# Kernel optimization log

Hardware: AMD Instinct MI355X
Metric: run time of the kernel (lower is better)

## Reference

```python
import jax, jax.numpy as jnp
import numpy as np

B, S, D, H = 2, 2048, 1024, 16
HD = D // H
EPS = 1e-5


def _layernorm(x, g, b):
    mu = jnp.mean(x, axis=-1, keepdims=True)
    var = jnp.mean(jnp.square(x - mu), axis=-1, keepdims=True)
    return (x - mu) * jax.lax.rsqrt(var + EPS) * g + b


def setup_inputs() -> dict:
    key = jax.random.key(0)
    ks = jax.random.split(key, 12)
    s = 1.0 / np.sqrt(D)
    return {
        "x": jax.random.normal(ks[0], (B, S, D), jnp.float32),
        "Wq": jax.random.uniform(ks[1], (D, D), jnp.float32, -s, s),
        "bq": jax.random.uniform(ks[2], (D,), jnp.float32, -s, s),
        "Wk": jax.random.uniform(ks[3], (D, D), jnp.float32, -s, s),
        "bk": jax.random.uniform(ks[4], (D,), jnp.float32, -s, s),
        "Wv": jax.random.uniform(ks[5], (D, D), jnp.float32, -s, s),
        "bv": jax.random.uniform(ks[6], (D,), jnp.float32, -s, s),
        "ln_g": jnp.ones((D,), jnp.float32),
        "ln_b": jnp.zeros((D,), jnp.float32),
        "W1": jax.random.uniform(ks[7], (D, D), jnp.float32, -s, s),
        "b1": jax.random.uniform(ks[8], (D,), jnp.float32, -s, s),
        "W2": jax.random.uniform(ks[9], (D, D), jnp.float32, -s, s),
        "b2": jax.random.uniform(ks[10], (D,), jnp.float32, -s, s),
    }


def reference(x, Wq, bq, Wk, bk, Wv, bv, ln_g, ln_b, W1, b1, W2, b2):
    # QKV projections (torch Linear: x @ W.T + b), split into heads -> [B,H,S,HD]
    q = (x @ Wq.T + bq).reshape(B, S, H, HD).transpose(0, 2, 1, 3)
    k = (x @ Wk.T + bk).reshape(B, S, H, HD).transpose(0, 2, 1, 3)
    v = (x @ Wv.T + bv).reshape(B, S, H, HD).transpose(0, 2, 1, 3)
    # Full score matrix [B,H,S,S] (faithful to unfused original)
    scores = jnp.einsum("bhqd,bhkd->bhqk", q, k) / np.sqrt(HD).astype(np.float32)
    attn = jax.nn.softmax(scores, axis=-1)  # dropout = identity (eval mode)
    ctx = jnp.einsum("bhqk,bhkd->bhqd", attn, v)
    ctx = ctx.transpose(0, 2, 1, 3).reshape(B, S, D)
    ctx = _layernorm(ctx + x, ln_g, ln_b)
    ffn = jax.nn.relu(ctx @ W1.T + b1) @ W2.T + b2
    return _layernorm(ffn + ctx, ln_g, ln_b)
```

## Files before the change

### kernel.cpp

```cpp
#include <hip/hip_runtime.h>
#include <stdint.h>

#define D_MODEL 1024
#define NHEAD   16
#define HDIM    64
#define BATCH   2
#define SEQ     2048
#define NTOK    (BATCH*SEQ)

typedef unsigned short u16;
typedef unsigned int   u32;
typedef __attribute__((ext_vector_type(8)))  short bf16x8;
typedef __attribute__((ext_vector_type(8)))  u16   u16x8;
typedef __attribute__((ext_vector_type(4)))  u16   u16x4;
typedef __attribute__((ext_vector_type(4)))  u32   u32x4;
typedef __attribute__((ext_vector_type(4)))  float f32x4;
typedef __attribute__((ext_vector_type(16))) float f32x16;

#if __has_builtin(__builtin_amdgcn_exp2f)
#define EXP2F __builtin_amdgcn_exp2f
#else
#define EXP2F exp2f
#endif

__device__ __forceinline__ u16 f2bf(float f) {
  uint32_t u = __float_as_uint(f);
  u += 0x7fffu + ((u >> 16) & 1u);
  return (u16)(u >> 16);
}

__device__ __forceinline__ void gl_lds16(const u16* g, u16* l) {
  __builtin_amdgcn_global_load_lds(
      (const __attribute__((address_space(1))) void*)g,
      (__attribute__((address_space(3))) void*)l, 16, 0, 0);
}

__device__ __forceinline__ u32 cvtpk(float lo, float hi) {
  u32 r;
  asm("v_cvt_pk_bf16_f32 %0, %1, %2" : "=v"(r) : "v"(lo), "v"(hi));
  return r;
}
__device__ __forceinline__ void pl32swap(u32& a, u32& b) {
  asm("v_permlane32_swap_b32 %0, %1" : "+v"(a), "+v"(b));
}

__device__ __forceinline__ f32x16 mfma32(bf16x8 a, bf16x8 b, f32x16 c) {
  return __builtin_amdgcn_mfma_f32_32x32x16_bf16(a, b, c, 0, 0, 0);
}

__global__ __launch_bounds__(256) void cvt_all(
    const float* __restrict__ x,  const float* __restrict__ Wq,
    const float* __restrict__ Wk, const float* __restrict__ Wv,
    const float* __restrict__ W1, const float* __restrict__ W2,
    const float* __restrict__ bq, const float* __restrict__ bk,
    const float* __restrict__ bv,
    u16* __restrict__ x_bf, u16* __restrict__ wqkv,
    u16* __restrict__ w1b,  u16* __restrict__ w2b,
    float* __restrict__ bqkv) {
  const int bid = blockIdx.x, t = threadIdx.x;
  if (bid == 4608) {
    for (int i = t; i < 3072; i += 256)
      bqkv[i] = i < 1024 ? bq[i] : (i < 2048 ? bk[i - 1024] : bv[i - 2048]);
    return;
  }
  const float* src; u16* dst; int off;
  if (bid < 2048)      { src = x;  dst = x_bf;            off = bid; }
  else if (bid < 2560) { src = Wq; dst = wqkv;            off = bid - 2048; }
  else if (bid < 3072) { src = Wk; dst = wqkv + (1 << 20); off = bid - 2560; }
  else if (bid < 3584) { src = Wv; dst = wqkv + (2 << 20); off = bid - 3072; }
  else if (bid < 4096) { src = W1; dst = w1b;             off = bid - 3584; }
  else                 { src = W2; dst = w2b;             off = bid - 4096; }
  const int i = (off * 256 + t) * 8;
  float4 a = *(const float4*)(src + i);
  float4 b = *(const float4*)(src + i + 4);
  u16x8 o;
  o[0] = f2bf(a.x); o[1] = f2bf(a.y); o[2] = f2bf(a.z); o[3] = f2bf(a.w);
  o[4] = f2bf(b.x); o[5] = f2bf(b.y); o[6] = f2bf(b.z); o[7] = f2bf(b.w);
  *(u16x8*)(dst + i) = o;
}

template <int EPI>
__global__ __launch_bounds__(256) void gemm_bt(const u16* __restrict__ A,
                                               const u16* __restrict__ B,
                                               const float* __restrict__ bias,
                                               void* __restrict__ C,
                                               int M, int N, int K) {
  __shared__ u16 a_lds[2][128 * 32];
  __shared__ u16 b_lds[2][128 * 32];
  const int t = threadIdx.x;
  const int l = t & 63;
  const int w = t >> 6;
  const int wr = w >> 1, wc = w & 1;
  const int gxn = N >> 7;
  const int cpx = gridDim.x >> 3;
  const int swz = (blockIdx.x & 7) * cpx + (blockIdx.x >> 3);
  const int bm = (swz / gxn) * 128, bn = (swz % gxn) * 128;
  const int fl = l & 15, fh = l >> 4;

  f32x4 acc[4][4] = {};

  const int row0 = t >> 2;
  const int row1 = (t + 256) >> 2;
  const int col0 = (t & 3) * 8;

#define GSTAGE(bb, kk)                                                         \
  gl_lds16(A + (size_t)(bm + row0) * K + (kk) + col0, &a_lds[bb][t * 8]);      \
  gl_lds16(A + (size_t)(bm + row1) * K + (kk) + col0,                          \
           &a_lds[bb][(t + 256) * 8]);                                         \
  gl_lds16(B + (size_t)(bn + row0) * K + (kk) + col0, &b_lds[bb][t * 8]);      \
  gl_lds16(B + (size_t)(bn + row1) * K + (kk) + col0,                          \
           &b_lds[bb][(t + 256) * 8]);

  GSTAGE(0, 0);
  __syncthreads();
  int cur = 0;

  for (int k0 = 0; k0 < K; k0 += 32) {
    if (k0 + 32 < K) { GSTAGE(cur ^ 1, k0 + 32); }

    bf16x8 af[4], bf[4];
#pragma unroll
    for (int mi = 0; mi < 4; ++mi)
      af[mi] = *(const bf16x8*)&a_lds[cur][(wr * 64 + mi * 16 + fl) * 32 + fh * 8];
#pragma unroll
    for (int ni = 0; ni < 4; ++ni)
      bf[ni] = *(const bf16x8*)&b_lds[cur][(wc * 64 + ni * 16 + fl) * 32 + fh * 8];
#pragma unroll
    for (int mi = 0; mi < 4; ++mi)
#pragma unroll
      for (int ni = 0; ni < 4; ++ni)
        acc[mi][ni] = __builtin_amdgcn_mfma_f32_16x16x32_bf16(
            af[mi], bf[ni], acc[mi][ni], 0, 0, 0);

    __syncthreads();
    cur ^= 1;
  }
#undef GSTAGE

#pragma unroll
  for (int mi = 0; mi < 4; ++mi) {
#pragma unroll
    for (int ni = 0; ni < 4; ++ni) {
      const int col = bn + wc * 64 + ni * 16 + fl;
      const float bv = bias ? bias[col] : 0.f;
#pragma unroll
      for (int r = 0; r < 4; ++r) {
        const int row = bm + wr * 64 + mi * 16 + fh * 4 + r;
        float v = acc[mi][ni][r] + bv;
        if (EPI == 0) {
          ((float*)C)[(size_t)row * N + col] = v;
        } else if (EPI == 1) {
          ((u16*)C)[(size_t)row * N + col] = f2bf(v);
        } else {
          ((u16*)C)[(size_t)row * N + col] = f2bf(fmaxf(v, 0.f));
        }
      }
    }
  }
}

__global__ __launch_bounds__(256) void transpose_v(const u16* __restrict__ qkv,
                                                   u16* __restrict__ vT) {
  __shared__ u16 tile[64][72];
  const int t = threadIdx.x;
  const int s0 = blockIdx.x * 64;
  const int bh = blockIdx.y, b = bh >> 4, h = bh & 15;
#pragma unroll
  for (int cc = 0; cc < 2; ++cc) {
    int idx = t + cc * 256, row = idx >> 3, c = idx & 7;
    *(bf16x8*)&tile[row][c * 8] = *(const bf16x8*)(
        qkv + (size_t)(b * SEQ + s0 + row) * 3072 + 2048 + h * 64 + c * 8);
  }
  __syncthreads();
#pragma unroll
  for (int cc = 0; cc < 2; ++cc) {
    int idx = t + cc * 256, drow = idx >> 3, c = idx & 7;
    u16x8 o;
#pragma unroll
    for (int j = 0; j < 8; ++j) o[j] = tile[c * 8 + j][drow];
    *(u16x8*)(vT + (size_t)(bh * 64 + drow) * SEQ + s0 + c * 8) = o;
  }
}

__global__ __launch_bounds__(256, 4) void attn_kernel(const u16* __restrict__ qkv,
                                                      const u16* __restrict__ vT,
                                                      float* __restrict__ ctx) {
  __shared__ u16 smem[4][64 * 64];
  __shared__ float mlbuf[2][2][32];

  const int t = threadIdx.x, l = t & 63, w = t >> 6;
  const int r0 = l & 31, hi = l >> 5, hib = hi * 16;
  const int qg = w >> 1, hfv = w & 1;

  const int id = blockIdx.x;
  const int swz = (id & 7) * 128 + (id >> 3);
  const int qblk = swz & 31;
  const int bh = swz >> 5;
  const int b = bh >> 4, h = bh & 15;
  const int q0 = qblk * 64;
  const size_t rowbase = (size_t)b * SEQ;

  bf16x8 qf[4];
#pragma unroll
  for (int kd = 0; kd < 4; ++kd)
    qf[kd] = *(const bf16x8*)(qkv +
        (rowbase + q0 + qg * 32 + r0) * 3072 + h * 64 + kd * 16 + hi * 8);

  f32x16 acc[2] = {};
  f32x16 lsum = {};
  const float C = 0.18033688011f;
  const float SM0 = 20.0f * C;
  const short ONEB = (short)0x3F80;
  const bf16x8 ones = {ONEB, ONEB, ONEB, ONEB, ONEB, ONEB, ONEB, ONEB};

  const u16* kb = smem[hfv * 2 + 0];
  const u16* vb = smem[hfv * 2 + 1];

  for (int s = 0; s < 16; ++s) {
    __syncthreads();
#pragma unroll
    for (int cc = 0; cc < 8; ++cc) {
      const int i = t + cc * 256;
      const int arr = i >> 9;
      const int j = i & 511;
      const int rr = j >> 3, cb = (j & 7) * 16;
      const int sc_ = cb ^ ((rr & 7) << 4);
      const int hv = arr >> 1;
      u16* dst = &smem[arr][j * 8];
      if ((arr & 1) == 0)
        gl_lds16(qkv + (rowbase + hv * 1024 + s * 64 + rr) * 3072 + 1024 +
                     h * 64 + (sc_ >> 1), dst);
      else
        gl_lds16(vT + ((size_t)bh * 64 + rr) * SEQ + hv * 1024 + s * 64 +
                     (sc_ >> 1), dst);
    }
    __syncthreads();

    f32x16 p0 = {}, p1 = {};
    __builtin_amdgcn_s_setprio(1);
#pragma unroll
    for (int kd = 0; kd < 4; ++kd) {
      const int cb = kd * 32 + hib;
      const uint8_t* pk = (const uint8_t*)kb;
      bf16x8 klo = *(const bf16x8*)(pk + r0 * 128 + (cb ^ ((r0 & 7) << 4)));
      bf16x8 khi = *(const bf16x8*)(pk + (r0 + 32) * 128 + (cb ^ ((r0 & 7) << 4)));
      p0 = mfma32(klo, qf[kd], p0);
      p1 = mfma32(khi, qf[kd], p1);
    }
    __builtin_amdgcn_s_setprio(0);

#pragma unroll
    for (int i = 0; i < 16; ++i) {
      p0[i] = EXP2F(fmaf(p0[i], C, -SM0));
      p1[i] = EXP2F(fmaf(p1[i], C, -SM0));
    }

    bf16x8 pb[4];
    {
      u32 c0, c1, c2, c3;
      u32x4 f;
      c0 = cvtpk(p0[0], p0[1]);   c1 = cvtpk(p0[2], p0[3]);
      c2 = cvtpk(p0[4], p0[5]);   c3 = cvtpk(p0[6], p0[7]);
      pl32swap(c0, c2); pl32swap(c1, c3);
      f[0] = c0; f[1] = c1; f[2] = c2; f[3] = c3; pb[0] = *(bf16x8*)&f;
      c0 = cvtpk(p0[8], p0[9]);   c1 = cvtpk(p0[10], p0[11]);
      c2 = cvtpk(p0[12], p0[13]); c3 = cvtpk(p0[14], p0[15]);
      pl32swap(c0, c2); pl32swap(c1, c3);
      f[0] = c0; f[1] = c1; f[2] = c2; f[3] = c3; pb[1] = *(bf16x8*)&f;
      c0 = cvtpk(p1[0], p1[1]);   c1 = cvtpk(p1[2], p1[3]);
      c2 = cvtpk(p1[4], p1[5]);   c3 = cvtpk(p1[6], p1[7]);
      pl32swap(c0, c2); pl32swap(c1, c3);
      f[0] = c0; f[1] = c1; f[2] = c2; f[3] = c3; pb[2] = *(bf16x8*)&f;
      c0 = cvtpk(p1[8], p1[9]);   c1 = cvtpk(p1[10], p1[11]);
      c2 = cvtpk(p1[12], p1[13]); c3 = cvtpk(p1[14], p1[15]);
      pl32swap(c0, c2); pl32swap(c1, c3);
      f[0] = c0; f[1] = c1; f[2] = c2; f[3] = c3; pb[3] = *(bf16x8*)&f;
    }

    __builtin_amdgcn_s_setprio(1);
#pragma unroll
    for (int ks = 0; ks < 4; ++ks)
      lsum = mfma32(ones, pb[ks], lsum);
#pragma unroll
    for (int dblk = 0; dblk < 2; ++dblk) {
#pragma unroll
      for (int ks = 0; ks < 4; ++ks) {
        const int rr = dblk * 32 + r0;
        const int cb = ks * 32 + hib;
        bf16x8 vf = *(const bf16x8*)((const uint8_t*)vb + rr * 128 +
                                     (cb ^ ((rr & 7) << 4)));
        acc[dblk] = mfma32(vf, pb[ks], acc[dblk]);
      }
    }
    __builtin_amdgcn_s_setprio(0);
  }

  if (hi == 0) mlbuf[qg][hfv][r0] = lsum[0];
  __syncthreads();

  float* os = (float*)smem + qg * 32 * 68;
  if (hfv == 0) {
#pragma unroll
    for (int dblk = 0; dblk < 2; ++dblk)
#pragma unroll
      for (int i = 0; i < 16; ++i) {
        const int d = dblk * 32 + (i & 3) + 8 * (i >> 2) + 4 * hi;
        os[r0 * 68 + d] = acc[dblk][i];
      }
  }
  __syncthreads();
  if (hfv == 1) {
#pragma unroll
    for (int dblk = 0; dblk < 2; ++dblk)
#pragma unroll
      for (int i = 0; i < 16; ++i) {
        const int d = dblk * 32 + (i & 3) + 8 * (i >> 2) + 4 * hi;
        os[r0 * 68 + d] += acc[dblk][i];
      }
#pragma unroll
    for (int it = 0; it < 8; ++it) {
      const int r = it * 4 + (l >> 4);
      const int c = (l & 15) * 4;
      const float inv = 1.f / (mlbuf[qg][0][r] + mlbuf[qg][1][r]);
      float4 v = *(const float4*)&os[r * 68 + c];
      v.x *= inv; v.y *= inv; v.z *= inv; v.w *= inv;
      *(float4*)&ctx[(rowbase + q0 + qg * 32 + r) * D_MODEL + h * 64 + c] = v;
    }
  }
}

__global__ __launch_bounds__(256) void ln_kernel(const float* __restrict__ a,
                                                 const float* __restrict__ res,
                                                 const float* __restrict__ g,
                                                 const float* __restrict__ bta,
                                                 float* __restrict__ outf,
                                                 u16* __restrict__ outb) {
  __shared__ float sbuf[4];
  const int t = threadIdx.x;
  const size_t row = blockIdx.x;
  const float4 va = *(const float4*)(a + row * 1024 + t * 4);
  const float4 vr = *(const float4*)(res + row * 1024 + t * 4);
  float v[4] = {va.x + vr.x, va.y + vr.y, va.z + vr.z, va.w + vr.w};
  float s = v[0] + v[1] + v[2] + v[3];
#pragma unroll
  for (int m = 32; m; m >>= 1) s += __shfl_xor(s, m, 64);
  if ((t & 63) == 0) sbuf[t >> 6] = s;
  __syncthreads();
  const float mean = (sbuf[0] + sbuf[1] + sbuf[2] + sbuf[3]) * (1.f / 1024.f);
  float q = 0.f;
#pragma unroll
  for (int i = 0; i < 4; ++i) { v[i] -= mean; q += v[i] * v[i]; }
#pragma unroll
  for (int m = 32; m; m >>= 1) q += __shfl_xor(q, m, 64);
  __syncthreads();
  if ((t & 63) == 0) sbuf[t >> 6] = q;
  __syncthreads();
  const float var = (sbuf[0] + sbuf[1] + sbuf[2] + sbuf[3]) * (1.f / 1024.f);
  const float rs = rsqrtf(var + 1e-5f);
  const float4 vg = *(const float4*)(g + t * 4);
  const float4 vb = *(const float4*)(bta + t * 4);
  float o[4];
  o[0] = v[0] * rs * vg.x + vb.x;
  o[1] = v[1] * rs * vg.y + vb.y;
  o[2] = v[2] * rs * vg.z + vb.z;
  o[3] = v[3] * rs * vg.w + vb.w;
  float4 of = {o[0], o[1], o[2], o[3]};
  *(float4*)(outf + row * 1024 + t * 4) = of;
  if (outb) {
    u16x4 ob;
#pragma unroll
    for (int i = 0; i < 4; ++i) ob[i] = f2bf(o[i]);
    *(u16x4*)(outb + row * 1024 + t * 4) = ob;
  }
}

extern "C" void kernel_launch(void* const* d_in, const int* in_sizes, int n_in,
                              void* d_out, int out_size, void* d_ws, size_t ws_size,
                              hipStream_t stream) {
  const float* x    = (const float*)d_in[0];
  const float* Wq   = (const float*)d_in[1];
  const float* bq   = (const float*)d_in[2];
  const float* Wk   = (const float*)d_in[3];
  const float* bk   = (const float*)d_in[4];
  const float* Wv   = (const float*)d_in[5];
  const float* bv   = (const float*)d_in[6];
  const float* ln_g = (const float*)d_in[7];
  const float* ln_b = (const float*)d_in[8];
  const float* W1   = (const float*)d_in[9];
  const float* b1   = (const float*)d_in[10];
  const float* W2   = (const float*)d_in[11];
  const float* b2   = (const float*)d_in[12];
  float* out = (float*)d_out;

  uint8_t* ws = (uint8_t*)d_ws;
  const size_t MB = 1 << 20;
  u16*   x_bf  = (u16*)  (ws + 0 * MB);
  u16*   wqkv  = (u16*)  (ws + 8 * MB);
  u16*   w1b   = (u16*)  (ws + 14 * MB);
  u16*   w2b   = (u16*)  (ws + 16 * MB);
  float* bqkv  = (float*)(ws + 18 * MB);
  u16*   qkv   = (u16*)  (ws + 19 * MB);
  u16*   vT    = (u16*)  (ws + 43 * MB);
  float* ctx   = (float*)(ws + 51 * MB);
  float* y     = (float*)(ws + 67 * MB);
  u16*   y_bf  = (u16*)  (ws + 83 * MB);
  u16*   h1    = (u16*)  (ws + 91 * MB);
  float* ffn   = (float*)(ws + 99 * MB);

  cvt_all<<<4609, 256, 0, stream>>>(x, Wq, Wk, Wv, W1, W2, bq, bk, bv,
                                    x_bf, wqkv, w1b, w2b, bqkv);
  gemm_bt<1><<<768, 256, 0, stream>>>(x_bf, wqkv, bqkv, qkv, NTOK, 3072, 1024);
  transpose_v<<<dim3(32, 32), 256, 0, stream>>>(qkv, vT);
  attn_kernel<<<1024, 256, 0, stream>>>(qkv, vT, ctx);
  ln_kernel<<<4096, 256, 0, stream>>>(ctx, x, ln_g, ln_b, y, y_bf);
  gemm_bt<2><<<256, 256, 0, stream>>>(y_bf, w1b, b1, h1, NTOK, 1024, 1024);
  gemm_bt<0><<<256, 256, 0, stream>>>(h1, w2b, b2, ffn, NTOK, 1024, 1024);
  ln_kernel<<<4096, 256, 0, stream>>>(ffn, y, ln_g, ln_b, out, nullptr);
}
```

Measured before the change: 270.5 us.

## Deepen GEMM global-to-LDS pipeline to four stages with explicit vmcnt waits

```diff
diff --git a/kernel.cpp b/kernel.cpp
--- a/kernel.cpp
+++ b/kernel.cpp
@@ -85,8 +85,8 @@
                                                const float* __restrict__ bias,
                                                void* __restrict__ C,
                                                int M, int N, int K) {
-  __shared__ u16 a_lds[2][128 * 32];
-  __shared__ u16 b_lds[2][128 * 32];
+  __shared__ u16 a_lds[4][128 * 32];
+  __shared__ u16 b_lds[4][128 * 32];
   const int t = threadIdx.x;
   const int l = t & 63;
   const int w = t >> 6;
@@ -96,46 +96,62 @@
   const int swz = (blockIdx.x & 7) * cpx + (blockIdx.x >> 3);
   const int bm = (swz / gxn) * 128, bn = (swz % gxn) * 128;
   const int fl = l & 15, fh = l >> 4;
+  const int NT = K >> 5;
 
   f32x4 acc[4][4] = {};
 
-  const int row0 = t >> 2;
-  const int row1 = (t + 256) >> 2;
-  const int col0 = (t & 3) * 8;
-
-#define GSTAGE(bb, kk)                                                         \
-  gl_lds16(A + (size_t)(bm + row0) * K + (kk) + col0, &a_lds[bb][t * 8]);      \
-  gl_lds16(A + (size_t)(bm + row1) * K + (kk) + col0,                          \
-           &a_lds[bb][(t + 256) * 8]);                                         \
-  gl_lds16(B + (size_t)(bn + row0) * K + (kk) + col0, &b_lds[bb][t * 8]);      \
-  gl_lds16(B + (size_t)(bn + row1) * K + (kk) + col0,                          \
-           &b_lds[bb][(t + 256) * 8]);
-
-  GSTAGE(0, 0);
-  __syncthreads();
-  int cur = 0;
-
-  for (int k0 = 0; k0 < K; k0 += 32) {
-    if (k0 + 32 < K) { GSTAGE(cur ^ 1, k0 + 32); }
-
-    bf16x8 af[4], bf[4];
-#pragma unroll
-    for (int mi = 0; mi < 4; ++mi)
-      af[mi] = *(const bf16x8*)&a_lds[cur][(wr * 64 + mi * 16 + fl) * 32 + fh * 8];
-#pragma unroll
-    for (int ni = 0; ni < 4; ++ni)
-      bf[ni] = *(const bf16x8*)&b_lds[cur][(wc * 64 + ni * 16 + fl) * 32 + fh * 8];
-#pragma unroll
-    for (int mi = 0; mi < 4; ++mi)
-#pragma unroll
-      for (int ni = 0; ni < 4; ++ni)
-        acc[mi][ni] = __builtin_amdgcn_mfma_f32_16x16x32_bf16(
-            af[mi], bf[ni], acc[mi][ni], 0, 0, 0);
-
-    __syncthreads();
-    cur ^= 1;
-  }
-#undef GSTAGE
+  const int srow = t >> 2;
+  const int scol = (t & 3) * 8;
+
+#define STG(bb, kt)                                                            \
+  {                                                                            \
+    gl_lds16(A + (size_t)(bm + srow) * K + (kt) * 32 + scol,                   \
+             &a_lds[bb][t * 8]);                                               \
+    gl_lds16(A + (size_t)(bm + 64 + srow) * K + (kt) * 32 + scol,              \
+             &a_lds[bb][(t + 256) * 8]);                                       \
+    gl_lds16(B + (size_t)(bn + srow) * K + (kt) * 32 + scol,                   \
+             &b_lds[bb][t * 8]);                                               \
+    gl_lds16(B + (size_t)(bn + 64 + srow) * K + (kt) * 32 + scol,              \
+             &b_lds[bb][(t + 256) * 8]);                                       \
+  }
+
+  STG(0, 0);
+  STG(1, 1);
+  STG(2, 2);
+
+#define KBODY(tt, VMS)                                                         \
+  {                                                                            \
+    __builtin_amdgcn_sched_barrier(0);                                         \
+    if ((tt) + 3 < NT) STG(((tt) + 3) & 3, (tt) + 3);                          \
+    asm volatile("s_waitcnt vmcnt(" VMS ")" ::: "memory");                     \
+    __builtin_amdgcn_sched_barrier(0);                                         \
+    __builtin_amdgcn_s_barrier();                                              \
+    __builtin_amdgcn_sched_barrier(0);                                         \
+    const u16* ap = a_lds[(tt) & 3];                                           \
+    const u16* bp = b_lds[(tt) & 3];                                           \
+    bf16x8 af[4], bf[4];                                                       \
+    _Pragma("unroll") for (int mi = 0; mi < 4; ++mi)                           \
+        af[mi] = *(const bf16x8*)&ap[(wr * 64 + mi * 16 + fl) * 32 + fh * 8];  \
+    _Pragma("unroll") for (int ni = 0; ni < 4; ++ni)                           \
+        bf[ni] = *(const bf16x8*)&bp[(wc * 64 + ni * 16 + fl) * 32 + fh * 8];  \
+    __builtin_amdgcn_s_setprio(1);                                             \
+    _Pragma("unroll") for (int mi = 0; mi < 4; ++mi)                           \
+        _Pragma("unroll") for (int ni = 0; ni < 4; ++ni)                       \
+            acc[mi][ni] = __builtin_amdgcn_mfma_f32_16x16x32_bf16(             \
+                af[mi], bf[ni], acc[mi][ni], 0, 0, 0);                         \
+    __builtin_amdgcn_s_setprio(0);                                             \
+    __builtin_amdgcn_sched_barrier(0);                                         \
+    asm volatile("s_waitcnt lgkmcnt(0)" ::: "memory");                         \
+    __builtin_amdgcn_sched_barrier(0);                                         \
+    __builtin_amdgcn_s_barrier();                                              \
+  }
+
+  for (int ti = 0; ti < NT - 3; ++ti) KBODY(ti, "12");
+  KBODY(NT - 3, "8");
+  KBODY(NT - 2, "4");
+  KBODY(NT - 1, "0");
+#undef KBODY
+#undef STG
 
 #pragma unroll
   for (int mi = 0; mi < 4; ++mi) {
```

Result: slower. 280.6 us (+3.7%).

## Fuse V transpose into QKV GEMM epilogue and add smaller-tile FFN GEMM

Applied to the files above, without the earlier changes.

```diff
diff --git a/kernel.cpp b/kernel.cpp
--- a/kernel.cpp
+++ b/kernel.cpp
@@ -84,6 +84,7 @@
                                                const u16* __restrict__ B,
                                                const float* __restrict__ bias,
                                                void* __restrict__ C,
+                                               u16* __restrict__ vT,
                                                int M, int N, int K) {
   __shared__ u16 a_lds[2][128 * 32];
   __shared__ u16 b_lds[2][128 * 32];
@@ -143,42 +144,105 @@
     for (int ni = 0; ni < 4; ++ni) {
       const int col = bn + wc * 64 + ni * 16 + fl;
       const float bv = bias ? bias[col] : 0.f;
+      const int rowb = bm + wr * 64 + mi * 16 + fh * 4;
+      if (EPI == 3 && col >= 2048) {
+        const int hd = col - 2048;
+        const int b_ = rowb >> 11, s_ = rowb & 2047;
+        u16x4 ob;
+#pragma unroll
+        for (int r = 0; r < 4; ++r) ob[r] = f2bf(acc[mi][ni][r] + bv);
+        *(u16x4*)(vT + ((size_t)(b_ * NHEAD + (hd >> 6)) * 64 + (hd & 63)) * SEQ
+                      + s_) = ob;
+      } else {
+#pragma unroll
+        for (int r = 0; r < 4; ++r) {
+          const int row = rowb + r;
+          float v = acc[mi][ni][r] + bv;
+          if (EPI == 0) {
+            ((float*)C)[(size_t)row * N + col] = v;
+          } else if (EPI == 2) {
+            ((u16*)C)[(size_t)row * N + col] = f2bf(fmaxf(v, 0.f));
+          } else {
+            ((u16*)C)[(size_t)row * N + col] = f2bf(v);
+          }
+        }
+      }
+    }
+  }
+}
+
+template <int EPI>
+__global__ __launch_bounds__(256) void gemm_ffn(const u16* __restrict__ A,
+                                                const u16* __restrict__ B,
+                                                const float* __restrict__ bias,
+                                                void* __restrict__ C,
+                                                int M, int N, int K) {
+  __shared__ u16 a_lds[2][64 * 32];
+  __shared__ u16 b_lds[2][128 * 32];
+  const int t = threadIdx.x;
+  const int l = t & 63;
+  const int w = t >> 6;
+  const int gxn = N >> 7;
+  const int cpx = gridDim.x >> 3;
+  const int swz = (blockIdx.x & 7) * cpx + (blockIdx.x >> 3);
+  const int bm = (swz / gxn) * 64, bn = (swz % gxn) * 128;
+  const int fl = l & 15, fh = l >> 4;
+
+  f32x4 acc[4][2] = {};
+
+  const int arow = t >> 2;
+  const int brow0 = t >> 2, brow1 = (t >> 2) + 64;
+  const int col0 = (t & 3) * 8;
+
+#define FSTAGE(bb, kk)                                                         \
+  gl_lds16(A + (size_t)(bm + arow) * K + (kk) + col0, &a_lds[bb][t * 8]);      \
+  gl_lds16(B + (size_t)(bn + brow0) * K + (kk) + col0, &b_lds[bb][t * 8]);     \
+  gl_lds16(B + (size_t)(bn + brow1) * K + (kk) + col0,                         \
+           &b_lds[bb][(t + 256) * 8]);
+
+  FSTAGE(0, 0);
+  __syncthreads();
+  int cur = 0;
+
+  for (int k0 = 0; k0 < K; k0 += 32) {
+    if (k0 + 32 < K) { FSTAGE(cur ^ 1, k0 + 32); }
+
+    bf16x8 af[4], bf[2];
+#pragma unroll
+    for (int mi = 0; mi < 4; ++mi)
+      af[mi] = *(const bf16x8*)&a_lds[cur][(mi * 16 + fl) * 32 + fh * 8];
+#pragma unroll
+    for (int ni = 0; ni < 2; ++ni)
+      bf[ni] = *(const bf16x8*)&b_lds[cur][(w * 32 + ni * 16 + fl) * 32 + fh * 8];
+#pragma unroll
+    for (int mi = 0; mi < 4; ++mi)
+#pragma unroll
+      for (int ni = 0; ni < 2; ++ni)
+        acc[mi][ni] = __builtin_amdgcn_mfma_f32_16x16x32_bf16(
+            af[mi], bf[ni], acc[mi][ni], 0, 0, 0);
+
+    __syncthreads();
+    cur ^= 1;
+  }
+#undef FSTAGE
+
+#pragma unroll
+  for (int mi = 0; mi < 4; ++mi) {
+#pragma unroll
+    for (int ni = 0; ni < 2; ++ni) {
+      const int col = bn + w * 32 + ni * 16 + fl;
+      const float bv = bias[col];
 #pragma unroll
       for (int r = 0; r < 4; ++r) {
-        const int row = bm + wr * 64 + mi * 16 + fh * 4 + r;
+        const int row = bm + mi * 16 + fh * 4 + r;
         float v = acc[mi][ni][r] + bv;
         if (EPI == 0) {
           ((float*)C)[(size_t)row * N + col] = v;
-        } else if (EPI == 1) {
-          ((u16*)C)[(size_t)row * N + col] = f2bf(v);
         } else {
           ((u16*)C)[(size_t)row * N + col] = f2bf(fmaxf(v, 0.f));
         }
       }
     }
-  }
-}
-
-__global__ __launch_bounds__(256) void transpose_v(const u16* __restrict__ qkv,
-                                                   u16* __restrict__ vT) {
-  __shared__ u16 tile[64][72];
-  const int t = threadIdx.x;
-  const int s0 = blockIdx.x * 64;
-  const int bh = blockIdx.y, b = bh >> 4, h = bh & 15;
-#pragma unroll
-  for (int cc = 0; cc < 2; ++cc) {
-    int idx = t + cc * 256, row = idx >> 3, c = idx & 7;
-    *(bf16x8*)&tile[row][c * 8] = *(const bf16x8*)(
-        qkv + (size_t)(b * SEQ + s0 + row) * 3072 + 2048 + h * 64 + c * 8);
-  }
-  __syncthreads();
-#pragma unroll
-  for (int cc = 0; cc < 2; ++cc) {
-    int idx = t + cc * 256, drow = idx >> 3, c = idx & 7;
-    u16x8 o;
-#pragma unroll
-    for (int j = 0; j < 8; ++j) o[j] = tile[c * 8 + j][drow];
-    *(u16x8*)(vT + (size_t)(bh * 64 + drow) * SEQ + s0 + c * 8) = o;
   }
 }
 
@@ -409,11 +473,11 @@
 
   cvt_all<<<4609, 256, 0, stream>>>(x, Wq, Wk, Wv, W1, W2, bq, bk, bv,
                                     x_bf, wqkv, w1b, w2b, bqkv);
-  gemm_bt<1><<<768, 256, 0, stream>>>(x_bf, wqkv, bqkv, qkv, NTOK, 3072, 1024);
-  transpose_v<<<dim3(32, 32), 256, 0, stream>>>(qkv, vT);
+  gemm_bt<3><<<768, 256, 0, stream>>>(x_bf, wqkv, bqkv, qkv, vT,
+                                      NTOK, 3072, 1024);
   attn_kernel<<<1024, 256, 0, stream>>>(qkv, vT, ctx);
   ln_kernel<<<4096, 256, 0, stream>>>(ctx, x, ln_g, ln_b, y, y_bf);
-  gemm_bt<2><<<256, 256, 0, stream>>>(y_bf, w1b, b1, h1, NTOK, 1024, 1024);
-  gemm_bt<0><<<256, 256, 0, stream>>>(h1, w2b, b2, ffn, NTOK, 1024, 1024);
+  gemm_ffn<2><<<512, 256, 0, stream>>>(y_bf, w1b, b1, h1, NTOK, 1024, 1024);
+  gemm_ffn<0><<<512, 256, 0, stream>>>(h1, w2b, b2, ffn, NTOK, 1024, 1024);
   ln_kernel<<<4096, 256, 0, stream>>>(ffn, y, ln_g, ln_b, out, nullptr);
 }
```

Result: faster. 252.0 us (-6.9%).
